# Performance work log

Measured on AMD Instinct MI355X. Metric: run time of the kernel, lower is better.

## Reference

```python
import jax, jax.numpy as jnp
import numpy as np

MAX_REL = 127  # default max_relative_position of NEZHA-style RelativePositionsEncoding


def rel_pos_encoding(L, d):
    """Clipped relative-distance sinusoidal encoding, shape [L, L, d]."""
    vocab = 2 * MAX_REL + 1
    pos = np.arange(vocab, dtype=np.float32)[:, None]
    i = np.arange(d)
    div = np.power(10000.0, (2 * (i // 2)) / d).astype(np.float32)
    ang = pos / div
    table = np.where(i % 2 == 0, np.sin(ang), np.cos(ang)).astype(np.float32)  # [vocab, d]
    dist = np.clip(np.arange(L)[None, :] - np.arange(L)[:, None], -MAX_REL, MAX_REL) + MAX_REL
    return jnp.asarray(table[dist])  # [L, L, d]


def setup_inputs() -> dict:
    key = jax.random.key(0)
    ks = jax.random.split(key, 5)
    B, L, H, C = 2, 256, 256, 5
    return {
        "hidden_state": jax.random.normal(ks[0], (B, L, H), dtype=jnp.float32),
        "mask": jnp.ones((B, L), dtype=jnp.int32),
        "Wh_w": jax.random.normal(ks[1], (4 * H, H), dtype=jnp.float32) * 0.02,
        "Wh_b": jax.random.normal(ks[2], (H,), dtype=jnp.float32) * 0.02,
        "Wo_w": jax.random.normal(ks[3], (H, C), dtype=jnp.float32) * 0.02,
        "Wo_b": jax.random.normal(ks[4], (C,), dtype=jnp.float32) * 0.02,
    }


def reference(hidden_state, mask, Wh_w, Wh_b, Wo_w, Wo_b):
    B, L, H = hidden_state.shape
    # Decompose Wh over the concat [end, start, end-start, end*start]:
    # Wh(cat) = end@(We+Wd) + start@(Ws-Wd) + (end*start)@Wm + rel@Wh + b  (exact, linearity)
    We, Ws, Wd, Wm = jnp.split(Wh_w, 4, axis=0)  # each [H, H]
    rel = rel_pos_encoding(L, 4 * H)                        # [L, L, 4H]
    rel_term = jnp.einsum('ijk,kh->ijh', rel, Wh_w)         # [L, L, H]
    a = hidden_state @ (We + Wd)                            # end-index contribution  [B, L, H]
    b = hidden_state @ (Ws - Wd)                            # start-index contribution [B, L, H]
    prod = hidden_state[:, :, None, :] * hidden_state[:, None, :, :]  # [B, L, L, H]
    pre = a[:, :, None, :] + b[:, None, :, :] + prod @ Wm + rel_term[None] + Wh_b
    hij = jnp.tanh(pre)                                     # [B, L, L, H]
    logits = hij @ Wo_w + Wo_b                              # [B, L, L, C]
    logits = jnp.transpose(logits, (0, 3, 1, 2))            # [B, C, L, L]
    m = mask.astype(bool)
    bad = (~m[:, None, :, None]) | (~m[:, None, None, :])
    logits = jnp.where(bad, -jnp.inf, logits)
    tri = jnp.tril(jnp.ones((L, L), logits.dtype), -1) * 1e12
    return logits - tri
```

## Files before the change

### kernel.cpp

```cpp
#include <hip/hip_runtime.h>
#include <math.h>

typedef _Float16 half8 __attribute__((ext_vector_type(8)));
typedef float floatx4 __attribute__((ext_vector_type(4)));

union U16 { uint4 u; half8 h; };

__global__ __launch_bounds__(512) void k_prep(
    const float* __restrict__ hs, const float* __restrict__ Wh,
    const float* __restrict__ Whb, const float* __restrict__ Wo,
    float* __restrict__ R, float* __restrict__ a, float* __restrict__ bv,
    uint4* __restrict__ WmT2, uint4* __restrict__ WoPk)
{
  __shared__ __align__(16) char pool[32768];
  int bid = blockIdx.x, tid = threadIdx.x;

  if (bid < 64) {
    float (*tbl)[4] = (float(*)[4])pool;
    float* part = (float*)(pool + 16384);
    int d0 = bid * 4;
    for (int idx = tid; idx < 4096; idx += 512) {
      int k = idx >> 2, dl = idx & 3;
      float e = (float)(k & ~1) * (1.0f / 1024.f);
      float div = powf(10000.f, e);
      float ang = (float)(d0 + dl) / div;
      tbl[k][dl] = (k & 1) ? cosf(ang) : sinf(ang);
    }
    __syncthreads();
    int h = tid & 255, s = tid >> 8;
    float acc[4] = {0.f, 0.f, 0.f, 0.f};
    for (int kk = 0; kk < 512; ++kk) {
      int k = s * 512 + kk;
      float wv = Wh[k * 256 + h];
      float4 tr = *(const float4*)&tbl[k][0];
      acc[0] = fmaf(tr.x, wv, acc[0]);
      acc[1] = fmaf(tr.y, wv, acc[1]);
      acc[2] = fmaf(tr.z, wv, acc[2]);
      acc[3] = fmaf(tr.w, wv, acc[3]);
    }
    if (s) {
#pragma unroll
      for (int dl = 0; dl < 4; ++dl) part[dl * 256 + h] = acc[dl];
    }
    __syncthreads();
    if (!s) {
#pragma unroll
      for (int dl = 0; dl < 4; ++dl)
        if (d0 + dl < 255)
          R[(d0 + dl) * 256 + h] = acc[dl] + part[dl * 256 + h];
    }

  } else if (bid < 128) {
    float (*xs)[8] = (float(*)[8])pool;
    float* pa = (float*)(pool + 8192);
    float* pb = (float*)(pool + 16384);
    int r0 = (bid - 64) * 8;
    for (int idx = tid; idx < 2048; idx += 512) {
      int k = idx & 255, r = idx >> 8;
      xs[k][r] = hs[(r0 + r) * 256 + k];
    }
    __syncthreads();
    int h = tid & 255, s = tid >> 8;
    float aa[8] = {0, 0, 0, 0, 0, 0, 0, 0}, bb[8] = {0, 0, 0, 0, 0, 0, 0, 0};
    for (int kk = 0; kk < 128; ++kk) {
      int k = s * 128 + kk;
      float we = Wh[k * 256 + h];
      float wsv = Wh[(256 + k) * 256 + h];
      float wd = Wh[(512 + k) * 256 + h];
      float wA = we + wd, wB = wsv - wd;
      float xr[8];
      *(float4*)&xr[0] = *(const float4*)&xs[k][0];
      *(float4*)&xr[4] = *(const float4*)&xs[k][4];
#pragma unroll
      for (int r = 0; r < 8; ++r) {
        aa[r] = fmaf(xr[r], wA, aa[r]);
        bb[r] = fmaf(xr[r], wB, bb[r]);
      }
    }
    if (s) {
#pragma unroll
      for (int r = 0; r < 8; ++r) { pa[r * 256 + h] = aa[r]; pb[r * 256 + h] = bb[r]; }
    }
    __syncthreads();
    if (!s) {
      float bias = Whb[h];
#pragma unroll
      for (int r = 0; r < 8; ++r) {
        a[(r0 + r) * 256 + h] = aa[r] + pa[r * 256 + h] + bias;
        bv[(r0 + r) * 256 + h] = bb[r] + pb[r * 256 + h];
      }
    }

  } else if (bid < 132) {
    _Float16 (*T)[256] = (_Float16(*)[256])pool;
    int q = bid - 128;
    for (int idx = tid; idx < 16384; idx += 512) {
      int k = idx >> 8, h = idx & 255;
      T[k][h] = (_Float16)Wh[(768 + q * 64 + k) * 256 + h];
    }
    __syncthreads();
    for (int gi = tid; gi < 2048; gi += 512) {
      int kbl = gi >> 8, h = gi & 255;
      U16 v;
#pragma unroll
      for (int e = 0; e < 8; ++e) v.h[e] = T[kbl * 8 + e][h];
      WmT2[(q * 8 + kbl) * 256 + h] = v.u;
    }

  } else {
    for (int gi = tid; gi < 512; gi += 512) {
      int kb = gi >> 4, c = gi & 15;
      U16 v;
#pragma unroll
      for (int e = 0; e < 8; ++e)
        v.h[e] = (c < 5) ? (_Float16)Wo[(kb * 8 + e) * 5 + c] : (_Float16)0.f;
      WoPk[gi] = v.u;
    }
  }
}

__global__ __launch_bounds__(256, 3) void k_main(
    const float* __restrict__ hs, const int* __restrict__ mask,
    const float* __restrict__ R, const float* __restrict__ a,
    const float* __restrict__ bvec, const uint4* __restrict__ WmT2,
    const uint4* __restrict__ WoPk, const float* __restrict__ Wob,
    float* __restrict__ out)
{
  __shared__ __align__(16) _Float16 As[2][32][264];

  int bid = blockIdx.x, tid = threadIdx.x;
  int jt = bid & 7, ig = (bid >> 3) & 127, b = bid >> 10;
  int i0 = ig * 2, j0 = jt * 32;
  int lane = tid & 63, w = tid >> 6;
  int c16 = lane & 15, quad = lane >> 4;
  const float* hsb = hs + (size_t)b * 65536;

  float av[2][4];
#pragma unroll
  for (int i2 = 0; i2 < 2; ++i2)
#pragma unroll
    for (int ht2 = 0; ht2 < 4; ++ht2)
      av[i2][ht2] = a[((size_t)(b * 256 + i0 + i2)) * 256 + 64 * w + 16 * ht2 + c16];

  floatx4 acc[2][2][4];
#pragma unroll
  for (int jt2 = 0; jt2 < 2; ++jt2) {
#pragma unroll
    for (int r = 0; r < 4; ++r) {
      int jg = j0 + jt2 * 16 + quad * 4 + r;
      float bvv[4];
#pragma unroll
      for (int ht2 = 0; ht2 < 4; ++ht2)
        bvv[ht2] = bvec[((size_t)(b * 256 + jg)) * 256 + 64 * w + 16 * ht2 + c16];
#pragma unroll
      for (int i2 = 0; i2 < 2; ++i2) {
        int dd = jg - (i0 + i2);
        dd = dd < -127 ? -127 : (dd > 127 ? 127 : dd);
        dd += 127;
        const float* rp = R + (size_t)dd * 256 + 64 * w;
#pragma unroll
        for (int ht2 = 0; ht2 < 4; ++ht2)
          acc[i2][jt2][ht2][r] = av[i2][ht2] + bvv[ht2] + rp[16 * ht2 + c16];
      }
    }
  }

  for (int idx = tid; idx < 2048; idx += 256) {
    int i2 = idx >> 10, j = (idx >> 5) & 31, k8 = (idx & 31) * 8;
    float4 xi0 = *(const float4*)(hsb + (i0 + i2) * 256 + k8);
    float4 xi1 = *(const float4*)(hsb + (i0 + i2) * 256 + k8 + 4);
    float4 xj0 = *(const float4*)(hsb + (j0 + j) * 256 + k8);
    float4 xj1 = *(const float4*)(hsb + (j0 + j) * 256 + k8 + 4);
    half8 p = {(_Float16)(xi0.x * xj0.x), (_Float16)(xi0.y * xj0.y),
               (_Float16)(xi0.z * xj0.z), (_Float16)(xi0.w * xj0.w),
               (_Float16)(xi1.x * xj1.x), (_Float16)(xi1.y * xj1.y),
               (_Float16)(xi1.z * xj1.z), (_Float16)(xi1.w * xj1.w)};
    *(half8*)(&As[i2][j][k8]) = p;
  }
  __syncthreads();

#pragma unroll 1
  for (int kc = 0; kc < 4; ++kc) {
#pragma unroll
    for (int ks = 0; ks < 2; ++ks) {
      int kb = kc * 8 + ks * 4 + quad;
      U16 bg[4];
#pragma unroll
      for (int ht2 = 0; ht2 < 4; ++ht2)
        bg[ht2].u = WmT2[kb * 256 + 64 * w + 16 * ht2 + c16];
      half8 af[2][2];
#pragma unroll
      for (int i2 = 0; i2 < 2; ++i2)
#pragma unroll
        for (int jt2 = 0; jt2 < 2; ++jt2)
          af[i2][jt2] =
              *(const half8*)(&As[i2][jt2 * 16 + c16][kc * 64 + ks * 32 + quad * 8]);
#pragma unroll
      for (int i2 = 0; i2 < 2; ++i2)
#pragma unroll
        for (int jt2 = 0; jt2 < 2; ++jt2)
#pragma unroll
          for (int ht2 = 0; ht2 < 4; ++ht2)
            acc[i2][jt2][ht2] = __builtin_amdgcn_mfma_f32_16x16x32_f16(
                af[i2][jt2], bg[ht2].h, acc[i2][jt2][ht2], 0, 0, 0);
    }
  }

  __syncthreads();

#pragma unroll
  for (int i2 = 0; i2 < 2; ++i2)
#pragma unroll
    for (int jt2 = 0; jt2 < 2; ++jt2)
#pragma unroll
      for (int ht2 = 0; ht2 < 4; ++ht2) {
        int hp = 64 * w + 16 * ht2 + c16;
#pragma unroll
        for (int r = 0; r < 4; ++r) {
          int jl = jt2 * 16 + quad * 4 + r;
          float x = acc[i2][jt2][ht2][r];
          float t = 1.f - 2.f / (__expf(2.f * x) + 1.f);
          As[i2][jl][hp] = (_Float16)t;
        }
      }
  __syncthreads();

  U16 wog[8];
#pragma unroll
  for (int s = 0; s < 8; ++s) wog[s].u = WoPk[(s * 4 + quad) * 16 + c16];
  floatx4 accE = {0.f, 0.f, 0.f, 0.f};
  int arow = 16 * w + c16;
  int i2a = arow >> 5, jla = arow & 31;
#pragma unroll
  for (int s = 0; s < 8; ++s) {
    half8 ae = *(const half8*)(&As[i2a][jla][s * 32 + quad * 8]);
    accE = __builtin_amdgcn_mfma_f32_16x16x32_f16(ae, wog[s].h, accE, 0, 0, 0);
  }

  const int* mb = mask + b * 256;
  float wob = (c16 < 5) ? Wob[c16] : 0.f;
#pragma unroll
  for (int r = 0; r < 4; ++r) {
    int grow = 16 * w + quad * 4 + r;
    int ii = i0 + (grow >> 5), jg = j0 + (grow & 31);
    float v = accE[r] + wob;
    if (!(mb[ii] && mb[jg])) v = -INFINITY;
    if (jg < ii) v -= 1e12f;
    if (c16 < 5) out[(((size_t)b * 5 + c16) * 256 + ii) * 256 + jg] = v;
  }
}

extern "C" void kernel_launch(void* const* d_in, const int* in_sizes, int n_in,
                              void* d_out, int out_size, void* d_ws, size_t ws_size,
                              hipStream_t stream) {
  const float* hs   = (const float*)d_in[0];
  const int*   mask = (const int*)d_in[1];
  const float* Wh_w = (const float*)d_in[2];
  const float* Wh_b = (const float*)d_in[3];
  const float* Wo_w = (const float*)d_in[4];
  const float* Wo_b = (const float*)d_in[5];

  char* ws = (char*)d_ws;
  float* R    = (float*)(ws + 0);
  float* a    = (float*)(ws + 262144);
  float* bv   = (float*)(ws + 786432);
  uint4* WmT2 = (uint4*)(ws + 1310720);
  uint4* WoPk = (uint4*)(ws + 1441792);

  k_prep<<<133, 512, 0, stream>>>(hs, Wh_w, Wh_b, Wo_w, R, a, bv, WmT2, WoPk);
  k_main<<<2048, 256, 0, stream>>>(hs, mask, R, a, bv, WmT2, WoPk, Wo_b,
                                   (float*)d_out);
}
```

Measured before the change: 131.8 us.

## Fold start-index and relative-position terms into MFMA via one-hot K extension

The per-element epilogue gathers of the b-vector and relative-position table are replaced by extending the GEMM's K dimension with one-hot columns in shared memory. Packed fp16 b-vector and relative-position rows then act as extra B-matrix blocks, so the MFMA loop does the adds. The loop also gains a software prefetch of the next B fragment, and prep now emits fp16-packed layouts. This removes scattered scalar global loads in exchange for three extra MFMA K-steps and fp16 rounding of the b and R terms.

```diff
diff --git a/kernel.cpp b/kernel.cpp
--- a/kernel.cpp
+++ b/kernel.cpp
@@ -9,18 +9,18 @@
 __global__ __launch_bounds__(512) void k_prep(
     const float* __restrict__ hs, const float* __restrict__ Wh,
     const float* __restrict__ Whb, const float* __restrict__ Wo,
-    float* __restrict__ R, float* __restrict__ a, float* __restrict__ bv,
-    uint4* __restrict__ WmT2, uint4* __restrict__ WoPk)
+    float* __restrict__ a, uint4* __restrict__ WmT2, uint4* __restrict__ bvPk,
+    uint4* __restrict__ R2Pk, uint4* __restrict__ WoPk)
 {
-  __shared__ __align__(16) char pool[32768];
+  __shared__ __align__(16) char pool[40960];
   int bid = blockIdx.x, tid = threadIdx.x;
 
-  if (bid < 64) {
-    float (*tbl)[4] = (float(*)[4])pool;
-    float* part = (float*)(pool + 16384);
-    int d0 = bid * 4;
-    for (int idx = tid; idx < 4096; idx += 512) {
-      int k = idx >> 2, dl = idx & 3;
+  if (bid < 32) {
+    float (*tbl)[8] = (float(*)[8])pool;
+    float* part = (float*)(pool + 32768);
+    int d0 = bid * 8;
+    for (int idx = tid; idx < 8192; idx += 512) {
+      int k = idx >> 3, dl = idx & 7;
       float e = (float)(k & ~1) * (1.0f / 1024.f);
       float div = powf(10000.f, e);
       float ang = (float)(d0 + dl) / div;
@@ -28,33 +28,36 @@
     }
     __syncthreads();
     int h = tid & 255, s = tid >> 8;
-    float acc[4] = {0.f, 0.f, 0.f, 0.f};
+    float acc[8] = {0, 0, 0, 0, 0, 0, 0, 0};
     for (int kk = 0; kk < 512; ++kk) {
       int k = s * 512 + kk;
       float wv = Wh[k * 256 + h];
-      float4 tr = *(const float4*)&tbl[k][0];
-      acc[0] = fmaf(tr.x, wv, acc[0]);
-      acc[1] = fmaf(tr.y, wv, acc[1]);
-      acc[2] = fmaf(tr.z, wv, acc[2]);
-      acc[3] = fmaf(tr.w, wv, acc[3]);
+      float tr[8];
+      *(float4*)&tr[0] = *(const float4*)&tbl[k][0];
+      *(float4*)&tr[4] = *(const float4*)&tbl[k][4];
+#pragma unroll
+      for (int dl = 0; dl < 8; ++dl) acc[dl] = fmaf(tr[dl], wv, acc[dl]);
     }
     if (s) {
 #pragma unroll
-      for (int dl = 0; dl < 4; ++dl) part[dl * 256 + h] = acc[dl];
+      for (int dl = 0; dl < 8; ++dl) part[dl * 256 + h] = acc[dl];
     }
     __syncthreads();
     if (!s) {
-#pragma unroll
-      for (int dl = 0; dl < 4; ++dl)
-        if (d0 + dl < 255)
-          R[(d0 + dl) * 256 + h] = acc[dl] + part[dl * 256 + h];
-    }
-
-  } else if (bid < 128) {
+      U16 v;
+#pragma unroll
+      for (int dl = 0; dl < 8; ++dl) {
+        float sum = acc[dl] + part[dl * 256 + h];
+        v.h[dl] = (d0 + dl < 255) ? (_Float16)sum : (_Float16)0.f;
+      }
+      R2Pk[bid * 256 + h] = v.u;
+    }
+
+  } else if (bid < 96) {
     float (*xs)[8] = (float(*)[8])pool;
     float* pa = (float*)(pool + 8192);
     float* pb = (float*)(pool + 16384);
-    int r0 = (bid - 64) * 8;
+    int r0 = (bid - 32) * 8;
     for (int idx = tid; idx < 2048; idx += 512) {
       int k = idx & 255, r = idx >> 8;
       xs[k][r] = hs[(r0 + r) * 256 + k];
@@ -84,16 +87,18 @@
     __syncthreads();
     if (!s) {
       float bias = Whb[h];
+      U16 v;
 #pragma unroll
       for (int r = 0; r < 8; ++r) {
         a[(r0 + r) * 256 + h] = aa[r] + pa[r * 256 + h] + bias;
-        bv[(r0 + r) * 256 + h] = bb[r] + pb[r * 256 + h];
-      }
-    }
-
-  } else if (bid < 132) {
+        v.h[r] = (_Float16)(bb[r] + pb[r * 256 + h]);
+      }
+      bvPk[(r0 >> 3) * 256 + h] = v.u;
+    }
+
+  } else if (bid < 100) {
     _Float16 (*T)[256] = (_Float16(*)[256])pool;
-    int q = bid - 128;
+    int q = bid - 96;
     for (int idx = tid; idx < 16384; idx += 512) {
       int k = idx >> 8, h = idx & 255;
       T[k][h] = (_Float16)Wh[(768 + q * 64 + k) * 256 + h];
@@ -108,25 +113,27 @@
     }
 
   } else {
-    for (int gi = tid; gi < 512; gi += 512) {
-      int kb = gi >> 4, c = gi & 15;
+    {
+      int kb = tid >> 4, c = tid & 15;
       U16 v;
 #pragma unroll
       for (int e = 0; e < 8; ++e)
         v.h[e] = (c < 5) ? (_Float16)Wo[(kb * 8 + e) * 5 + c] : (_Float16)0.f;
-      WoPk[gi] = v.u;
-    }
+      WoPk[tid] = v.u;
+    }
+    uint4 z = {0, 0, 0, 0};
+    for (int idx = tid; idx < 2048; idx += 512) R2Pk[8192 + idx] = z;
   }
 }
 
 __global__ __launch_bounds__(256, 3) void k_main(
     const float* __restrict__ hs, const int* __restrict__ mask,
-    const float* __restrict__ R, const float* __restrict__ a,
-    const float* __restrict__ bvec, const uint4* __restrict__ WmT2,
+    const float* __restrict__ a, const uint4* __restrict__ WmT2,
+    const uint4* __restrict__ bvPk, const uint4* __restrict__ R2Pk,
     const uint4* __restrict__ WoPk, const float* __restrict__ Wob,
     float* __restrict__ out)
 {
-  __shared__ __align__(16) _Float16 As[2][32][264];
+  __shared__ __align__(16) _Float16 As[2][32][360];
 
   int bid = blockIdx.x, tid = threadIdx.x;
   int jt = bid & 7, ig = (bid >> 3) & 127, b = bid >> 10;
@@ -135,75 +142,99 @@
   int c16 = lane & 15, quad = lane >> 4;
   const float* hsb = hs + (size_t)b * 65536;
 
+  int ddmin = j0 - i0 - 1 + 127;
+  ddmin = ddmin < 0 ? 0 : (ddmin > 254 ? 254 : ddmin);
+  int g0 = ddmin & ~7;
+
   float av[2][4];
 #pragma unroll
   for (int i2 = 0; i2 < 2; ++i2)
 #pragma unroll
     for (int ht2 = 0; ht2 < 4; ++ht2)
       av[i2][ht2] = a[((size_t)(b * 256 + i0 + i2)) * 256 + 64 * w + 16 * ht2 + c16];
-
   floatx4 acc[2][2][4];
 #pragma unroll
-  for (int jt2 = 0; jt2 < 2; ++jt2) {
-#pragma unroll
-    for (int r = 0; r < 4; ++r) {
-      int jg = j0 + jt2 * 16 + quad * 4 + r;
-      float bvv[4];
+  for (int i2 = 0; i2 < 2; ++i2)
+#pragma unroll
+    for (int jt2 = 0; jt2 < 2; ++jt2)
 #pragma unroll
       for (int ht2 = 0; ht2 < 4; ++ht2)
-        bvv[ht2] = bvec[((size_t)(b * 256 + jg)) * 256 + 64 * w + 16 * ht2 + c16];
-#pragma unroll
-      for (int i2 = 0; i2 < 2; ++i2) {
-        int dd = jg - (i0 + i2);
-        dd = dd < -127 ? -127 : (dd > 127 ? 127 : dd);
-        dd += 127;
-        const float* rp = R + (size_t)dd * 256 + 64 * w;
+        acc[i2][jt2][ht2] = (floatx4){av[i2][ht2], av[i2][ht2], av[i2][ht2], av[i2][ht2]};
+
+  {
+    uint4 z = {0, 0, 0, 0};
+    for (int e = tid; e < 768; e += 256) {
+      int row = e / 12, q = e - row * 12;
+      *(uint4*)(&As[row >> 5][row & 31][256 + q * 8]) = z;
+    }
+  }
+
+  {
+    int k8 = (tid & 31) * 8, jb = tid >> 5;
+#pragma unroll
+    for (int i2 = 0; i2 < 2; ++i2) {
+      float4 xi0 = *(const float4*)(hsb + (i0 + i2) * 256 + k8);
+      float4 xi1 = *(const float4*)(hsb + (i0 + i2) * 256 + k8 + 4);
+#pragma unroll
+      for (int m = 0; m < 4; ++m) {
+        int j = jb + 8 * m;
+        float4 xj0 = *(const float4*)(hsb + (j0 + j) * 256 + k8);
+        float4 xj1 = *(const float4*)(hsb + (j0 + j) * 256 + k8 + 4);
+        half8 p = {(_Float16)(xi0.x * xj0.x), (_Float16)(xi0.y * xj0.y),
+                   (_Float16)(xi0.z * xj0.z), (_Float16)(xi0.w * xj0.w),
+                   (_Float16)(xi1.x * xj1.x), (_Float16)(xi1.y * xj1.y),
+                   (_Float16)(xi1.z * xj1.z), (_Float16)(xi1.w * xj1.w)};
+        *(half8*)(&As[i2][j][k8]) = p;
+      }
+    }
+  }
+  __syncthreads();
+
+  if (tid < 64) {
+    int i2 = tid >> 5, jl = tid & 31;
+    int dd = j0 + jl - i0 - i2;
+    dd = dd < -127 ? -127 : (dd > 127 ? 127 : dd);
+    dd += 127;
+    As[i2][jl][256 + jl] = (_Float16)1.f;
+    As[i2][jl][288 + (dd - g0)] = (_Float16)1.f;
+  }
+  __syncthreads();
+
+  const int hbase = 64 * w + c16;
+  const uint4* bvBase = bvPk + (((b * 256 + j0) >> 3) + quad) * 256;
+  const uint4* rBase = R2Pk + ((g0 >> 3) + quad) * 256;
+  U16 bg[4], bgn[4];
+#pragma unroll
+  for (int ht2 = 0; ht2 < 4; ++ht2)
+    bg[ht2].u = WmT2[quad * 256 + hbase + 16 * ht2];
+#pragma unroll 1
+  for (int kb32 = 0; kb32 < 11; ++kb32) {
+    if (kb32 < 10) {
+      const uint4* bp;
+      int nk = kb32 + 1;
+      if (nk < 8)       bp = WmT2 + (nk * 4 + quad) * 256;
+      else if (nk == 8) bp = bvBase;
+      else              bp = rBase + (nk - 9) * 1024;
+#pragma unroll
+      for (int ht2 = 0; ht2 < 4; ++ht2) bgn[ht2].u = bp[hbase + 16 * ht2];
+    }
+    half8 af[2][2];
+#pragma unroll
+    for (int i2 = 0; i2 < 2; ++i2)
+#pragma unroll
+      for (int jt2 = 0; jt2 < 2; ++jt2)
+        af[i2][jt2] =
+            *(const half8*)(&As[i2][jt2 * 16 + c16][kb32 * 32 + quad * 8]);
+#pragma unroll
+    for (int i2 = 0; i2 < 2; ++i2)
+#pragma unroll
+      for (int jt2 = 0; jt2 < 2; ++jt2)
 #pragma unroll
         for (int ht2 = 0; ht2 < 4; ++ht2)
-          acc[i2][jt2][ht2][r] = av[i2][ht2] + bvv[ht2] + rp[16 * ht2 + c16];
-      }
-    }
-  }
-
-  for (int idx = tid; idx < 2048; idx += 256) {
-    int i2 = idx >> 10, j = (idx >> 5) & 31, k8 = (idx & 31) * 8;
-    float4 xi0 = *(const float4*)(hsb + (i0 + i2) * 256 + k8);
-    float4 xi1 = *(const float4*)(hsb + (i0 + i2) * 256 + k8 + 4);
-    float4 xj0 = *(const float4*)(hsb + (j0 + j) * 256 + k8);
-    float4 xj1 = *(const float4*)(hsb + (j0 + j) * 256 + k8 + 4);
-    half8 p = {(_Float16)(xi0.x * xj0.x), (_Float16)(xi0.y * xj0.y),
-               (_Float16)(xi0.z * xj0.z), (_Float16)(xi0.w * xj0.w),
-               (_Float16)(xi1.x * xj1.x), (_Float16)(xi1.y * xj1.y),
-               (_Float16)(xi1.z * xj1.z), (_Float16)(xi1.w * xj1.w)};
-    *(half8*)(&As[i2][j][k8]) = p;
-  }
-  __syncthreads();
-
-#pragma unroll 1
-  for (int kc = 0; kc < 4; ++kc) {
-#pragma unroll
-    for (int ks = 0; ks < 2; ++ks) {
-      int kb = kc * 8 + ks * 4 + quad;
-      U16 bg[4];
-#pragma unroll
-      for (int ht2 = 0; ht2 < 4; ++ht2)
-        bg[ht2].u = WmT2[kb * 256 + 64 * w + 16 * ht2 + c16];
-      half8 af[2][2];
-#pragma unroll
-      for (int i2 = 0; i2 < 2; ++i2)
-#pragma unroll
-        for (int jt2 = 0; jt2 < 2; ++jt2)
-          af[i2][jt2] =
-              *(const half8*)(&As[i2][jt2 * 16 + c16][kc * 64 + ks * 32 + quad * 8]);
-#pragma unroll
-      for (int i2 = 0; i2 < 2; ++i2)
-#pragma unroll
-        for (int jt2 = 0; jt2 < 2; ++jt2)
-#pragma unroll
-          for (int ht2 = 0; ht2 < 4; ++ht2)
-            acc[i2][jt2][ht2] = __builtin_amdgcn_mfma_f32_16x16x32_f16(
-                af[i2][jt2], bg[ht2].h, acc[i2][jt2][ht2], 0, 0, 0);
-    }
+          acc[i2][jt2][ht2] = __builtin_amdgcn_mfma_f32_16x16x32_f16(
+              af[i2][jt2], bg[ht2].h, acc[i2][jt2][ht2], 0, 0, 0);
+#pragma unroll
+    for (int t = 0; t < 4; ++t) bg[t] = bgn[t];
   }
 
   __syncthreads();
@@ -261,13 +292,13 @@
   const float* Wo_b = (const float*)d_in[5];
 
   char* ws = (char*)d_ws;
-  float* R    = (float*)(ws + 0);
-  float* a    = (float*)(ws + 262144);
-  float* bv   = (float*)(ws + 786432);
-  uint4* WmT2 = (uint4*)(ws + 1310720);
-  uint4* WoPk = (uint4*)(ws + 1441792);
-
-  k_prep<<<133, 512, 0, stream>>>(hs, Wh_w, Wh_b, Wo_w, R, a, bv, WmT2, WoPk);
-  k_main<<<2048, 256, 0, stream>>>(hs, mask, R, a, bv, WmT2, WoPk, Wo_b,
+  float* a    = (float*)(ws + 0);
+  uint4* WmT2 = (uint4*)(ws + 524288);
+  uint4* bvPk = (uint4*)(ws + 655360);
+  uint4* R2Pk = (uint4*)(ws + 917504);
+  uint4* WoPk = (uint4*)(ws + 1081344);
+
+  k_prep<<<101, 512, 0, stream>>>(hs, Wh_w, Wh_b, Wo_w, a, WmT2, bvPk, R2Pk, WoPk);
+  k_main<<<2048, 256, 0, stream>>>(hs, mask, a, WmT2, bvPk, R2Pk, WoPk, Wo_b,
                                    (float*)d_out);
 }
```

Result: slower. 151.3 us (+14.8%).

## Double block size to 512 threads, split H across 8 waves, prefetch weights

Applied to the files above, without the earlier changes.

The main kernel now launches 512 threads per block, and each of the 8 waves owns 32 hidden columns instead of 64. This halves the per-wave accumulators and B-fragment registers so more waves can be resident. The K loop is flattened to 8 steps, with the Wm fragments for the next step loaded ahead in registers. The product tile is built with packed cvt_pkrtz conversions and reuses the loaded i-rows. The final Wo projection runs only on the first 4 waves, leaving the other half idle during the epilogue.

```diff
diff --git a/kernel.cpp b/kernel.cpp
--- a/kernel.cpp
+++ b/kernel.cpp
@@ -2,9 +2,10 @@
 #include <math.h>
 
 typedef _Float16 half8 __attribute__((ext_vector_type(8)));
+typedef __fp16 fp16x2 __attribute__((ext_vector_type(2)));
 typedef float floatx4 __attribute__((ext_vector_type(4)));
 
-union U16 { uint4 u; half8 h; };
+union U16 { uint4 u; half8 h; fp16x2 p[4]; };
 
 __global__ __launch_bounds__(512) void k_prep(
     const float* __restrict__ hs, const float* __restrict__ Wh,
@@ -108,18 +109,16 @@
     }
 
   } else {
-    for (int gi = tid; gi < 512; gi += 512) {
-      int kb = gi >> 4, c = gi & 15;
-      U16 v;
-#pragma unroll
-      for (int e = 0; e < 8; ++e)
-        v.h[e] = (c < 5) ? (_Float16)Wo[(kb * 8 + e) * 5 + c] : (_Float16)0.f;
-      WoPk[gi] = v.u;
-    }
+    int kb = tid >> 4, c = tid & 15;
+    U16 v;
+#pragma unroll
+    for (int e = 0; e < 8; ++e)
+      v.h[e] = (c < 5) ? (_Float16)Wo[(kb * 8 + e) * 5 + c] : (_Float16)0.f;
+    WoPk[tid] = v.u;
   }
 }
 
-__global__ __launch_bounds__(256, 3) void k_main(
+__global__ __launch_bounds__(512, 6) void k_main(
     const float* __restrict__ hs, const int* __restrict__ mask,
     const float* __restrict__ R, const float* __restrict__ a,
     const float* __restrict__ bvec, const uint4* __restrict__ WmT2,
@@ -135,77 +134,90 @@
   int c16 = lane & 15, quad = lane >> 4;
   const float* hsb = hs + (size_t)b * 65536;
 
-  float av[2][4];
-#pragma unroll
-  for (int i2 = 0; i2 < 2; ++i2)
-#pragma unroll
-    for (int ht2 = 0; ht2 < 4; ++ht2)
-      av[i2][ht2] = a[((size_t)(b * 256 + i0 + i2)) * 256 + 64 * w + 16 * ht2 + c16];
-
-  floatx4 acc[2][2][4];
+  {
+    int k8 = (tid & 31) * 8, rb = tid >> 5;
+    float4 xi00 = *(const float4*)(hsb + i0 * 256 + k8);
+    float4 xi01 = *(const float4*)(hsb + i0 * 256 + k8 + 4);
+    float4 xi10 = *(const float4*)(hsb + (i0 + 1) * 256 + k8);
+    float4 xi11 = *(const float4*)(hsb + (i0 + 1) * 256 + k8 + 4);
+#pragma unroll
+    for (int m = 0; m < 4; ++m) {
+      int row = rb + 16 * m;
+      int i2 = row >> 5, j = row & 31;
+      float4 xj0 = *(const float4*)(hsb + (j0 + j) * 256 + k8);
+      float4 xj1 = *(const float4*)(hsb + (j0 + j) * 256 + k8 + 4);
+      float4 y0 = i2 ? xi10 : xi00;
+      float4 y1 = i2 ? xi11 : xi01;
+      U16 v;
+      v.p[0] = __builtin_amdgcn_cvt_pkrtz(y0.x * xj0.x, y0.y * xj0.y);
+      v.p[1] = __builtin_amdgcn_cvt_pkrtz(y0.z * xj0.z, y0.w * xj0.w);
+      v.p[2] = __builtin_amdgcn_cvt_pkrtz(y1.x * xj1.x, y1.y * xj1.y);
+      v.p[3] = __builtin_amdgcn_cvt_pkrtz(y1.z * xj1.z, y1.w * xj1.w);
+      *(uint4*)(&As[i2][j][k8]) = v.u;
+    }
+  }
+
+  int hb = 32 * w + c16;
+  float av0[2], av1[2];
+#pragma unroll
+  for (int i2 = 0; i2 < 2; ++i2) {
+    const float* ap = a + ((size_t)(b * 256 + i0 + i2)) * 256 + hb;
+    av0[i2] = ap[0];
+    av1[i2] = ap[16];
+  }
+  floatx4 acc[2][2][2];
 #pragma unroll
   for (int jt2 = 0; jt2 < 2; ++jt2) {
 #pragma unroll
     for (int r = 0; r < 4; ++r) {
       int jg = j0 + jt2 * 16 + quad * 4 + r;
-      float bvv[4];
-#pragma unroll
-      for (int ht2 = 0; ht2 < 4; ++ht2)
-        bvv[ht2] = bvec[((size_t)(b * 256 + jg)) * 256 + 64 * w + 16 * ht2 + c16];
+      const float* bp = bvec + ((size_t)(b * 256 + jg)) * 256 + hb;
+      float b0 = bp[0], b1 = bp[16];
 #pragma unroll
       for (int i2 = 0; i2 < 2; ++i2) {
-        int dd = jg - (i0 + i2);
+        int dd = jg - i0 - i2;
         dd = dd < -127 ? -127 : (dd > 127 ? 127 : dd);
         dd += 127;
-        const float* rp = R + (size_t)dd * 256 + 64 * w;
-#pragma unroll
-        for (int ht2 = 0; ht2 < 4; ++ht2)
-          acc[i2][jt2][ht2][r] = av[i2][ht2] + bvv[ht2] + rp[16 * ht2 + c16];
-      }
-    }
-  }
-
-  for (int idx = tid; idx < 2048; idx += 256) {
-    int i2 = idx >> 10, j = (idx >> 5) & 31, k8 = (idx & 31) * 8;
-    float4 xi0 = *(const float4*)(hsb + (i0 + i2) * 256 + k8);
-    float4 xi1 = *(const float4*)(hsb + (i0 + i2) * 256 + k8 + 4);
-    float4 xj0 = *(const float4*)(hsb + (j0 + j) * 256 + k8);
-    float4 xj1 = *(const float4*)(hsb + (j0 + j) * 256 + k8 + 4);
-    half8 p = {(_Float16)(xi0.x * xj0.x), (_Float16)(xi0.y * xj0.y),
-               (_Float16)(xi0.z * xj0.z), (_Float16)(xi0.w * xj0.w),
-               (_Float16)(xi1.x * xj1.x), (_Float16)(xi1.y * xj1.y),
-               (_Float16)(xi1.z * xj1.z), (_Float16)(xi1.w * xj1.w)};
-    *(half8*)(&As[i2][j][k8]) = p;
+        const float* rp = R + (size_t)dd * 256 + hb;
+        acc[i2][jt2][0][r] = av0[i2] + b0 + rp[0];
+        acc[i2][jt2][1][r] = av1[i2] + b1 + rp[16];
+      }
+    }
   }
   __syncthreads();
 
+  U16 bg0, bg1, bn0, bn1;
+  {
+    const uint4* wp = WmT2 + quad * 256 + hb;
+    bg0.u = wp[0];
+    bg1.u = wp[16];
+  }
 #pragma unroll 1
-  for (int kc = 0; kc < 4; ++kc) {
-#pragma unroll
-    for (int ks = 0; ks < 2; ++ks) {
-      int kb = kc * 8 + ks * 4 + quad;
-      U16 bg[4];
-#pragma unroll
-      for (int ht2 = 0; ht2 < 4; ++ht2)
-        bg[ht2].u = WmT2[kb * 256 + 64 * w + 16 * ht2 + c16];
-      half8 af[2][2];
-#pragma unroll
-      for (int i2 = 0; i2 < 2; ++i2)
-#pragma unroll
-        for (int jt2 = 0; jt2 < 2; ++jt2)
-          af[i2][jt2] =
-              *(const half8*)(&As[i2][jt2 * 16 + c16][kc * 64 + ks * 32 + quad * 8]);
-#pragma unroll
-      for (int i2 = 0; i2 < 2; ++i2)
-#pragma unroll
-        for (int jt2 = 0; jt2 < 2; ++jt2)
-#pragma unroll
-          for (int ht2 = 0; ht2 < 4; ++ht2)
-            acc[i2][jt2][ht2] = __builtin_amdgcn_mfma_f32_16x16x32_f16(
-                af[i2][jt2], bg[ht2].h, acc[i2][jt2][ht2], 0, 0, 0);
-    }
-  }
-
+  for (int ks = 0; ks < 8; ++ks) {
+    if (ks < 7) {
+      const uint4* wp = WmT2 + ((ks + 1) * 4 + quad) * 256 + hb;
+      bn0.u = wp[0];
+      bn1.u = wp[16];
+    }
+    half8 af[2][2];
+#pragma unroll
+    for (int i2 = 0; i2 < 2; ++i2)
+#pragma unroll
+      for (int jt2 = 0; jt2 < 2; ++jt2)
+        af[i2][jt2] =
+            *(const half8*)(&As[i2][jt2 * 16 + c16][ks * 32 + quad * 8]);
+#pragma unroll
+    for (int i2 = 0; i2 < 2; ++i2)
+#pragma unroll
+      for (int jt2 = 0; jt2 < 2; ++jt2) {
+        acc[i2][jt2][0] = __builtin_amdgcn_mfma_f32_16x16x32_f16(
+            af[i2][jt2], bg0.h, acc[i2][jt2][0], 0, 0, 0);
+        acc[i2][jt2][1] = __builtin_amdgcn_mfma_f32_16x16x32_f16(
+            af[i2][jt2], bg1.h, acc[i2][jt2][1], 0, 0, 0);
+      }
+    bg0 = bn0;
+    bg1 = bn1;
+  }
   __syncthreads();
 
 #pragma unroll
@@ -213,40 +225,41 @@
 #pragma unroll
     for (int jt2 = 0; jt2 < 2; ++jt2)
 #pragma unroll
-      for (int ht2 = 0; ht2 < 4; ++ht2) {
-        int hp = 64 * w + 16 * ht2 + c16;
+      for (int ct2 = 0; ct2 < 2; ++ct2) {
+        int hp = hb + 16 * ct2;
 #pragma unroll
         for (int r = 0; r < 4; ++r) {
           int jl = jt2 * 16 + quad * 4 + r;
-          float x = acc[i2][jt2][ht2][r];
+          float x = acc[i2][jt2][ct2][r];
           float t = 1.f - 2.f / (__expf(2.f * x) + 1.f);
           As[i2][jl][hp] = (_Float16)t;
         }
       }
   __syncthreads();
 
-  U16 wog[8];
-#pragma unroll
-  for (int s = 0; s < 8; ++s) wog[s].u = WoPk[(s * 4 + quad) * 16 + c16];
-  floatx4 accE = {0.f, 0.f, 0.f, 0.f};
-  int arow = 16 * w + c16;
-  int i2a = arow >> 5, jla = arow & 31;
-#pragma unroll
-  for (int s = 0; s < 8; ++s) {
-    half8 ae = *(const half8*)(&As[i2a][jla][s * 32 + quad * 8]);
-    accE = __builtin_amdgcn_mfma_f32_16x16x32_f16(ae, wog[s].h, accE, 0, 0, 0);
-  }
-
-  const int* mb = mask + b * 256;
-  float wob = (c16 < 5) ? Wob[c16] : 0.f;
-#pragma unroll
-  for (int r = 0; r < 4; ++r) {
-    int grow = 16 * w + quad * 4 + r;
-    int ii = i0 + (grow >> 5), jg = j0 + (grow & 31);
-    float v = accE[r] + wob;
-    if (!(mb[ii] && mb[jg])) v = -INFINITY;
-    if (jg < ii) v -= 1e12f;
-    if (c16 < 5) out[(((size_t)b * 5 + c16) * 256 + ii) * 256 + jg] = v;
+  if (w < 4) {
+    U16 wog[8];
+#pragma unroll
+    for (int s = 0; s < 8; ++s) wog[s].u = WoPk[(s * 4 + quad) * 16 + c16];
+    floatx4 accE = {0.f, 0.f, 0.f, 0.f};
+    int arow = 16 * w + c16;
+    int i2a = arow >> 5, jla = arow & 31;
+#pragma unroll
+    for (int s = 0; s < 8; ++s) {
+      half8 ae = *(const half8*)(&As[i2a][jla][s * 32 + quad * 8]);
+      accE = __builtin_amdgcn_mfma_f32_16x16x32_f16(ae, wog[s].h, accE, 0, 0, 0);
+    }
+    const int* mb = mask + b * 256;
+    float wob = (c16 < 5) ? Wob[c16] : 0.f;
+#pragma unroll
+    for (int r = 0; r < 4; ++r) {
+      int grow = 16 * w + quad * 4 + r;
+      int ii = i0 + (grow >> 5), jg = j0 + (grow & 31);
+      float v = accE[r] + wob;
+      if (!(mb[ii] && mb[jg])) v = -INFINITY;
+      if (jg < ii) v -= 1e12f;
+      if (c16 < 5) out[(((size_t)b * 5 + c16) * 256 + ii) * 256 + jg] = v;
+    }
   }
 }
 
@@ -268,6 +281,6 @@
   uint4* WoPk = (uint4*)(ws + 1441792);
 
   k_prep<<<133, 512, 0, stream>>>(hs, Wh_w, Wh_b, Wo_w, R, a, bv, WmT2, WoPk);
-  k_main<<<2048, 256, 0, stream>>>(hs, mask, R, a, bv, WmT2, WoPk, Wo_b,
+  k_main<<<2048, 512, 0, stream>>>(hs, mask, R, a, bv, WmT2, WoPk, Wo_b,
                                    (float*)d_out);
 }
```

After: 132.2 us. No clear change (+0.3%).

## Switch pairwise GEMM to FP8 MFMA with register-resident weights and per-row blocks

Applied to the files above, without the earlier changes.

The Wm projection is now quantized to FP8 with a scale of 16, and so are the pairwise products hs_i*hs_j. The main GEMM uses 16x16x32 fp8 MFMA, and the scale is undone in the epilogue. Each 512-thread block now handles one query row i and loops over eight 32-column j tiles. It keeps its slice of Wm in registers and stages Wo in LDS, so the weights are reused across tiles instead of being reloaded per block. This cuts global weight traffic and doubles MFMA throughput. In exchange it loses accuracy from FP8 rounding and runs fewer, larger blocks, with two barriers per j tile.

```diff
diff --git a/kernel.cpp b/kernel.cpp
--- a/kernel.cpp
+++ b/kernel.cpp
@@ -2,6 +2,7 @@
 #include <math.h>
 
 typedef _Float16 half8 __attribute__((ext_vector_type(8)));
+typedef __fp16 fp16x2 __attribute__((ext_vector_type(2)));
 typedef float floatx4 __attribute__((ext_vector_type(4)));
 
 union U16 { uint4 u; half8 h; };
@@ -10,7 +11,7 @@
     const float* __restrict__ hs, const float* __restrict__ Wh,
     const float* __restrict__ Whb, const float* __restrict__ Wo,
     float* __restrict__ R, float* __restrict__ a, float* __restrict__ bv,
-    uint4* __restrict__ WmT2, uint4* __restrict__ WoPk)
+    unsigned long long* __restrict__ WmPk, uint4* __restrict__ WoPk)
 {
   __shared__ __align__(16) char pool[32768];
   int bid = blockIdx.x, tid = threadIdx.x;
@@ -92,161 +93,171 @@
     }
 
   } else if (bid < 132) {
-    _Float16 (*T)[256] = (_Float16(*)[256])pool;
     int q = bid - 128;
-    for (int idx = tid; idx < 16384; idx += 512) {
-      int k = idx >> 8, h = idx & 255;
-      T[k][h] = (_Float16)Wh[(768 + q * 64 + k) * 256 + h];
-    }
-    __syncthreads();
-    for (int gi = tid; gi < 2048; gi += 512) {
-      int kbl = gi >> 8, h = gi & 255;
-      U16 v;
-#pragma unroll
-      for (int e = 0; e < 8; ++e) v.h[e] = T[kbl * 8 + e][h];
-      WmT2[(q * 8 + kbl) * 256 + h] = v.u;
+#pragma unroll
+    for (int v = 0; v < 4; ++v) {
+      int idx = v * 512 + tid;
+      int k8 = q * 8 + (idx >> 8);
+      int h = idx & 255;
+      const float* src = Wh + (768 + k8 * 8) * 256 + h;
+      float f[8];
+#pragma unroll
+      for (int e = 0; e < 8; ++e) f[e] = src[e * 256] * 16.f;
+      int lo = __builtin_amdgcn_cvt_pk_fp8_f32(f[0], f[1], 0, false);
+      lo = __builtin_amdgcn_cvt_pk_fp8_f32(f[2], f[3], lo, true);
+      int hi = __builtin_amdgcn_cvt_pk_fp8_f32(f[4], f[5], 0, false);
+      hi = __builtin_amdgcn_cvt_pk_fp8_f32(f[6], f[7], hi, true);
+      WmPk[k8 * 256 + h] =
+          ((unsigned long long)(unsigned)hi << 32) | (unsigned)lo;
     }
 
   } else {
-    for (int gi = tid; gi < 512; gi += 512) {
-      int kb = gi >> 4, c = gi & 15;
-      U16 v;
-#pragma unroll
-      for (int e = 0; e < 8; ++e)
-        v.h[e] = (c < 5) ? (_Float16)Wo[(kb * 8 + e) * 5 + c] : (_Float16)0.f;
-      WoPk[gi] = v.u;
-    }
+    int k8 = tid >> 4, c = tid & 15;
+    U16 v;
+#pragma unroll
+    for (int e = 0; e < 8; ++e)
+      v.h[e] = (c < 5) ? (_Float16)Wo[(k8 * 8 + e) * 5 + c] : (_Float16)0.f;
+    WoPk[tid] = v.u;
   }
 }
 
-__global__ __launch_bounds__(256, 3) void k_main(
+__global__ __launch_bounds__(512, 4) void k_main(
     const float* __restrict__ hs, const int* __restrict__ mask,
     const float* __restrict__ R, const float* __restrict__ a,
-    const float* __restrict__ bvec, const uint4* __restrict__ WmT2,
+    const float* __restrict__ bvec,
+    const unsigned long long* __restrict__ WmPk,
     const uint4* __restrict__ WoPk, const float* __restrict__ Wob,
     float* __restrict__ out)
 {
-  __shared__ __align__(16) _Float16 As[2][32][264];
+  __shared__ __align__(16) unsigned char As[32][272];
+  __shared__ __align__(16) __fp16 Ps[32][272];
+  __shared__ __align__(16) uint4 WoL[512];
 
   int bid = blockIdx.x, tid = threadIdx.x;
-  int jt = bid & 7, ig = (bid >> 3) & 127, b = bid >> 10;
-  int i0 = ig * 2, j0 = jt * 32;
+  int b = bid >> 8, i = bid & 255;
   int lane = tid & 63, w = tid >> 6;
   int c16 = lane & 15, quad = lane >> 4;
   const float* hsb = hs + (size_t)b * 65536;
 
-  float av[2][4];
-#pragma unroll
-  for (int i2 = 0; i2 < 2; ++i2)
-#pragma unroll
-    for (int ht2 = 0; ht2 < 4; ++ht2)
-      av[i2][ht2] = a[((size_t)(b * 256 + i0 + i2)) * 256 + 64 * w + 16 * ht2 + c16];
-
-  floatx4 acc[2][2][4];
-#pragma unroll
-  for (int jt2 = 0; jt2 < 2; ++jt2) {
-#pragma unroll
-    for (int r = 0; r < 4; ++r) {
-      int jg = j0 + jt2 * 16 + quad * 4 + r;
-      float bvv[4];
-#pragma unroll
-      for (int ht2 = 0; ht2 < 4; ++ht2)
-        bvv[ht2] = bvec[((size_t)(b * 256 + jg)) * 256 + 64 * w + 16 * ht2 + c16];
-#pragma unroll
-      for (int i2 = 0; i2 < 2; ++i2) {
-        int dd = jg - (i0 + i2);
+  WoL[tid] = WoPk[tid];
+
+  long long bg[8][2];
+#pragma unroll
+  for (int ks = 0; ks < 8; ++ks)
+#pragma unroll
+    for (int ct = 0; ct < 2; ++ct)
+      bg[ks][ct] =
+          (long long)WmPk[(ks * 4 + quad) * 256 + 32 * w + 16 * ct + c16];
+
+  float av[2];
+#pragma unroll
+  for (int ct = 0; ct < 2; ++ct)
+    av[ct] = a[((size_t)(b * 256 + i)) * 256 + 32 * w + 16 * ct + c16];
+
+  const int* mb = mask + b * 256;
+  int mi = mb[i];
+  float wob = (c16 < 5) ? Wob[c16] : 0.f;
+
+  int arow = tid >> 4;
+  int kg = (tid & 15) * 16;
+  const float* xip = hsb + i * 256 + kg;
+
+#pragma unroll 1
+  for (int jt = 0; jt < 8; ++jt) {
+    int j0 = jt * 32;
+
+    {
+      const float* xjp = hsb + (j0 + arow) * 256 + kg;
+      float4 xi0 = *(const float4*)(xip);
+      float4 xi1 = *(const float4*)(xip + 4);
+      float4 xi2 = *(const float4*)(xip + 8);
+      float4 xi3 = *(const float4*)(xip + 12);
+      float4 xj0 = *(const float4*)(xjp);
+      float4 xj1 = *(const float4*)(xjp + 4);
+      float4 xj2 = *(const float4*)(xjp + 8);
+      float4 xj3 = *(const float4*)(xjp + 12);
+      int w0 = __builtin_amdgcn_cvt_pk_fp8_f32(xi0.x * xj0.x, xi0.y * xj0.y, 0, false);
+      w0 = __builtin_amdgcn_cvt_pk_fp8_f32(xi0.z * xj0.z, xi0.w * xj0.w, w0, true);
+      int w1 = __builtin_amdgcn_cvt_pk_fp8_f32(xi1.x * xj1.x, xi1.y * xj1.y, 0, false);
+      w1 = __builtin_amdgcn_cvt_pk_fp8_f32(xi1.z * xj1.z, xi1.w * xj1.w, w1, true);
+      int w2 = __builtin_amdgcn_cvt_pk_fp8_f32(xi2.x * xj2.x, xi2.y * xj2.y, 0, false);
+      w2 = __builtin_amdgcn_cvt_pk_fp8_f32(xi2.z * xj2.z, xi2.w * xj2.w, w2, true);
+      int w3 = __builtin_amdgcn_cvt_pk_fp8_f32(xi3.x * xj3.x, xi3.y * xj3.y, 0, false);
+      w3 = __builtin_amdgcn_cvt_pk_fp8_f32(xi3.z * xj3.z, xi3.w * xj3.w, w3, true);
+      uint4 pk = {(unsigned)w0, (unsigned)w1, (unsigned)w2, (unsigned)w3};
+      *(uint4*)(&As[arow][kg]) = pk;
+    }
+
+    float cv[2][2][4];
+#pragma unroll
+    for (int rt = 0; rt < 2; ++rt)
+#pragma unroll
+      for (int r = 0; r < 4; ++r) {
+        int jg = j0 + rt * 16 + quad * 4 + r;
+        int dd = jg - i;
         dd = dd < -127 ? -127 : (dd > 127 ? 127 : dd);
         dd += 127;
-        const float* rp = R + (size_t)dd * 256 + 64 * w;
-#pragma unroll
-        for (int ht2 = 0; ht2 < 4; ++ht2)
-          acc[i2][jt2][ht2][r] = av[i2][ht2] + bvv[ht2] + rp[16 * ht2 + c16];
-      }
-    }
-  }
-
-  for (int idx = tid; idx < 2048; idx += 256) {
-    int i2 = idx >> 10, j = (idx >> 5) & 31, k8 = (idx & 31) * 8;
-    float4 xi0 = *(const float4*)(hsb + (i0 + i2) * 256 + k8);
-    float4 xi1 = *(const float4*)(hsb + (i0 + i2) * 256 + k8 + 4);
-    float4 xj0 = *(const float4*)(hsb + (j0 + j) * 256 + k8);
-    float4 xj1 = *(const float4*)(hsb + (j0 + j) * 256 + k8 + 4);
-    half8 p = {(_Float16)(xi0.x * xj0.x), (_Float16)(xi0.y * xj0.y),
-               (_Float16)(xi0.z * xj0.z), (_Float16)(xi0.w * xj0.w),
-               (_Float16)(xi1.x * xj1.x), (_Float16)(xi1.y * xj1.y),
-               (_Float16)(xi1.z * xj1.z), (_Float16)(xi1.w * xj1.w)};
-    *(half8*)(&As[i2][j][k8]) = p;
-  }
-  __syncthreads();
-
-#pragma unroll 1
-  for (int kc = 0; kc < 4; ++kc) {
-#pragma unroll
-    for (int ks = 0; ks < 2; ++ks) {
-      int kb = kc * 8 + ks * 4 + quad;
-      U16 bg[4];
-#pragma unroll
-      for (int ht2 = 0; ht2 < 4; ++ht2)
-        bg[ht2].u = WmT2[kb * 256 + 64 * w + 16 * ht2 + c16];
-      half8 af[2][2];
-#pragma unroll
-      for (int i2 = 0; i2 < 2; ++i2)
-#pragma unroll
-        for (int jt2 = 0; jt2 < 2; ++jt2)
-          af[i2][jt2] =
-              *(const half8*)(&As[i2][jt2 * 16 + c16][kc * 64 + ks * 32 + quad * 8]);
-#pragma unroll
-      for (int i2 = 0; i2 < 2; ++i2)
-#pragma unroll
-        for (int jt2 = 0; jt2 < 2; ++jt2)
-#pragma unroll
-          for (int ht2 = 0; ht2 < 4; ++ht2)
-            acc[i2][jt2][ht2] = __builtin_amdgcn_mfma_f32_16x16x32_f16(
-                af[i2][jt2], bg[ht2].h, acc[i2][jt2][ht2], 0, 0, 0);
-    }
-  }
-
-  __syncthreads();
-
-#pragma unroll
-  for (int i2 = 0; i2 < 2; ++i2)
-#pragma unroll
-    for (int jt2 = 0; jt2 < 2; ++jt2)
-#pragma unroll
-      for (int ht2 = 0; ht2 < 4; ++ht2) {
-        int hp = 64 * w + 16 * ht2 + c16;
-#pragma unroll
-        for (int r = 0; r < 4; ++r) {
-          int jl = jt2 * 16 + quad * 4 + r;
-          float x = acc[i2][jt2][ht2][r];
-          float t = 1.f - 2.f / (__expf(2.f * x) + 1.f);
-          As[i2][jl][hp] = (_Float16)t;
+        const float* bp = bvec + ((size_t)(b * 256 + jg)) * 256 + 32 * w + c16;
+        const float* rp = R + dd * 256 + 32 * w + c16;
+#pragma unroll
+        for (int ct = 0; ct < 2; ++ct)
+          cv[rt][ct][r] = av[ct] + bp[16 * ct] + rp[16 * ct];
+      }
+    __syncthreads();
+
+    floatx4 acc[2][2];
+#pragma unroll
+    for (int rt = 0; rt < 2; ++rt)
+#pragma unroll
+      for (int ct = 0; ct < 2; ++ct)
+        acc[rt][ct] = (floatx4){0.f, 0.f, 0.f, 0.f};
+#pragma unroll
+    for (int ks = 0; ks < 8; ++ks) {
+      long long a0 = *(const long long*)(&As[c16][ks * 32 + quad * 8]);
+      long long a1 = *(const long long*)(&As[16 + c16][ks * 32 + quad * 8]);
+      acc[0][0] = __builtin_amdgcn_mfma_f32_16x16x32_fp8_fp8(a0, bg[ks][0], acc[0][0], 0, 0, 0);
+      acc[0][1] = __builtin_amdgcn_mfma_f32_16x16x32_fp8_fp8(a0, bg[ks][1], acc[0][1], 0, 0, 0);
+      acc[1][0] = __builtin_amdgcn_mfma_f32_16x16x32_fp8_fp8(a1, bg[ks][0], acc[1][0], 0, 0, 0);
+      acc[1][1] = __builtin_amdgcn_mfma_f32_16x16x32_fp8_fp8(a1, bg[ks][1], acc[1][1], 0, 0, 0);
+    }
+
+#pragma unroll
+    for (int rt = 0; rt < 2; ++rt)
+#pragma unroll
+      for (int ct = 0; ct < 2; ++ct) {
+        int col = 32 * w + 16 * ct + c16;
+#pragma unroll
+        for (int r = 0; r < 4; r += 2) {
+          int row = rt * 16 + quad * 4 + r;
+          float p0 = fmaf(acc[rt][ct][r], 0.0625f, cv[rt][ct][r]);
+          float p1 = fmaf(acc[rt][ct][r + 1], 0.0625f, cv[rt][ct][r + 1]);
+          float t0 = 1.f - 2.f * __builtin_amdgcn_rcpf(__expf(2.f * p0) + 1.f);
+          float t1 = 1.f - 2.f * __builtin_amdgcn_rcpf(__expf(2.f * p1) + 1.f);
+          fp16x2 pk = __builtin_amdgcn_cvt_pkrtz(t0, t1);
+          Ps[row][col] = pk.x;
+          Ps[row + 1][col] = pk.y;
         }
       }
-  __syncthreads();
-
-  U16 wog[8];
-#pragma unroll
-  for (int s = 0; s < 8; ++s) wog[s].u = WoPk[(s * 4 + quad) * 16 + c16];
-  floatx4 accE = {0.f, 0.f, 0.f, 0.f};
-  int arow = 16 * w + c16;
-  int i2a = arow >> 5, jla = arow & 31;
-#pragma unroll
-  for (int s = 0; s < 8; ++s) {
-    half8 ae = *(const half8*)(&As[i2a][jla][s * 32 + quad * 8]);
-    accE = __builtin_amdgcn_mfma_f32_16x16x32_f16(ae, wog[s].h, accE, 0, 0, 0);
-  }
-
-  const int* mb = mask + b * 256;
-  float wob = (c16 < 5) ? Wob[c16] : 0.f;
-#pragma unroll
-  for (int r = 0; r < 4; ++r) {
-    int grow = 16 * w + quad * 4 + r;
-    int ii = i0 + (grow >> 5), jg = j0 + (grow & 31);
-    float v = accE[r] + wob;
-    if (!(mb[ii] && mb[jg])) v = -INFINITY;
-    if (jg < ii) v -= 1e12f;
-    if (c16 < 5) out[(((size_t)b * 5 + c16) * 256 + ii) * 256 + jg] = v;
+    __syncthreads();
+
+    if (w < 2) {
+      floatx4 accE = {0.f, 0.f, 0.f, 0.f};
+#pragma unroll
+      for (int ks = 0; ks < 8; ++ks) {
+        half8 pa = *(const half8*)(&Ps[w * 16 + c16][ks * 32 + quad * 8]);
+        U16 wv;
+        wv.u = WoL[(ks * 4 + quad) * 16 + c16];
+        accE = __builtin_amdgcn_mfma_f32_16x16x32_f16(pa, wv.h, accE, 0, 0, 0);
+      }
+#pragma unroll
+      for (int r = 0; r < 4; ++r) {
+        int jg = j0 + w * 16 + quad * 4 + r;
+        float v = accE[r] + wob;
+        if (!(mi && mb[jg])) v = -__builtin_inff();
+        if (jg < i) v -= 1e12f;
+        if (c16 < 5) out[(((size_t)b * 5 + c16) * 256 + i) * 256 + jg] = v;
+      }
+    }
   }
 }
 
@@ -264,10 +275,10 @@
   float* R    = (float*)(ws + 0);
   float* a    = (float*)(ws + 262144);
   float* bv   = (float*)(ws + 786432);
-  uint4* WmT2 = (uint4*)(ws + 1310720);
-  uint4* WoPk = (uint4*)(ws + 1441792);
-
-  k_prep<<<133, 512, 0, stream>>>(hs, Wh_w, Wh_b, Wo_w, R, a, bv, WmT2, WoPk);
-  k_main<<<2048, 256, 0, stream>>>(hs, mask, R, a, bv, WmT2, WoPk, Wo_b,
-                                   (float*)d_out);
+  unsigned long long* WmPk = (unsigned long long*)(ws + 1310720);
+  uint4* WoPk = (uint4*)(ws + 1376256);
+
+  k_prep<<<133, 512, 0, stream>>>(hs, Wh_w, Wh_b, Wo_w, R, a, bv, WmPk, WoPk);
+  k_main<<<512, 512, 0, stream>>>(hs, mask, R, a, bv, WmPk, WoPk, Wo_b,
+                                  (float*)d_out);
 }
```

Measured after the change: 145.4 us. +10.3%, slower.
